# Performance work log

Hardware: AMD Instinct MI355X
Metric: run time of the kernel (lower is better)

## Reference

```python
import jax, jax.numpy as jnp
import numpy as np

N_NODES = 200000
N_GRAPHS = 4000


def _sage_conv(x, src, dst, W_l, b_l, W_r, num_nodes):
    # PyG SAGEConv (aggr='mean'): out = lin_l(mean_{j in N(i)} x_j) + lin_r(x_i)
    msg_sum = jax.ops.segment_sum(x[src], dst, num_segments=num_nodes)      # [N, d]
    deg = jax.ops.segment_sum(jnp.ones_like(src, dtype=x.dtype), dst,
                              num_segments=num_nodes)                       # [N]
    mean_nbr = msg_sum / jnp.maximum(deg, 1.0)[:, None]
    return mean_nbr @ W_l.T + b_l + x @ W_r.T


def setup_inputs() -> dict:
    key = jax.random.key(0)
    ks = jax.random.split(key, 10)
    in_ch, hid, out = 32, 64, 2
    E = 3200000
    x = jax.random.normal(ks[0], (N_NODES, in_ch), dtype=jnp.float32)
    edge_index = jax.random.randint(ks[1], (2, E), 0, N_NODES, dtype=jnp.int64)
    batch = jnp.sort(jax.random.randint(ks[2], (N_NODES,), 0, N_GRAPHS, dtype=jnp.int64))

    def glorot(k, shape):
        lim = 1.0 / np.sqrt(shape[1])
        return jax.random.uniform(k, shape, jnp.float32, -lim, lim)

    return {
        "x": x,
        "edge_index": edge_index,
        "batch": batch,
        "W1_l": glorot(ks[3], (hid, in_ch)),
        "b1": jnp.zeros((hid,), jnp.float32),
        "W1_r": glorot(ks[4], (hid, in_ch)),
        "W2_l": glorot(ks[5], (hid, hid)),
        "b2": jnp.zeros((hid,), jnp.float32),
        "W2_r": glorot(ks[6], (hid, hid)),
        "W_lin": glorot(ks[7], (out, hid)),
        "b_lin": jnp.zeros((out,), jnp.float32),
    }


def reference(x, edge_index, batch, W1_l, b1, W1_r, W2_l, b2, W2_r, W_lin, b_lin):
    src, dst = edge_index[0], edge_index[1]
    h = jax.nn.relu(_sage_conv(x, src, dst, W1_l, b1, W1_r, N_NODES))
    h = jax.nn.relu(_sage_conv(h, src, dst, W2_l, b2, W2_r, N_NODES))
    # global_mean_pool over graph ids
    pool_sum = jax.ops.segment_sum(h, batch, num_segments=N_GRAPHS)          # [G, 64]
    cnt = jax.ops.segment_sum(jnp.ones_like(batch, dtype=h.dtype), batch,
                              num_segments=N_GRAPHS)                          # [G]
    pooled = pool_sum / jnp.maximum(cnt, 1.0)[:, None]
    return pooled @ W_lin.T + b_lin
```

## Files before the change

### kernel.cpp

```cpp
#include <hip/hip_runtime.h>
#include <hip/hip_bf16.h>


#define WS_ALIGN 64
#define EPB 4096
#define BSHIFT 8
#define BNODES 256
#define BCAP 6144
#define MAXNB 1024

typedef short bf16x8 __attribute__((ext_vector_type(8)));
typedef float f32x4 __attribute__((ext_vector_type(4)));

__device__ inline unsigned short f2bf(float f) {
    unsigned u = __float_as_uint(f);
    return (unsigned short)((u + 0x7fffu + ((u >> 16) & 1u)) >> 16);
}

__device__ inline void acc8(const uint4 u, float* a) {
    a[0] += __uint_as_float(u.x << 16);
    a[1] += __uint_as_float(u.x & 0xffff0000u);
    a[2] += __uint_as_float(u.y << 16);
    a[3] += __uint_as_float(u.y & 0xffff0000u);
    a[4] += __uint_as_float(u.z << 16);
    a[5] += __uint_as_float(u.z & 0xffff0000u);
    a[6] += __uint_as_float(u.w << 16);
    a[7] += __uint_as_float(u.w & 0xffff0000u);
}


__global__ void prep_kernel(const float* __restrict__ x, unsigned short* __restrict__ xb,
                            const float* __restrict__ W1_l, const float* __restrict__ W1_r,
                            const float* __restrict__ W2_l, const float* __restrict__ W2_r,
                            unsigned short* __restrict__ whi1, unsigned short* __restrict__ whi2,
                            int* __restrict__ bucketCursor, float* __restrict__ pool,
                            int N, int NB, int G, int total4) {
    const int gid = blockIdx.x * blockDim.x + threadIdx.x;
    if (gid < total4) {
        const float4 v = reinterpret_cast<const float4*>(x)[gid];
        ushort4 o;
        o.x = f2bf(v.x); o.y = f2bf(v.y); o.z = f2bf(v.z); o.w = f2bf(v.w);
        reinterpret_cast<ushort4*>(xb)[gid] = o;
    }
    if (gid < NB) bucketCursor[gid] = gid * BCAP;
    if (gid < G * 64) pool[gid] = 0.0f;
    if (gid < 64 * 64) {
        const int o = gid >> 6, k = gid & 63;
        const float v = (k < 32) ? W1_l[o * 32 + k] : W1_r[o * 32 + (k - 32)];
        whi1[gid] = f2bf(v);
    }
    if (gid < 64 * 128) {
        const int o = gid >> 7, k = gid & 127;
        const float v = (k < 64) ? W2_l[o * 64 + k] : W2_r[o * 64 + (k - 64)];
        whi2[gid] = f2bf(v);
    }
}


__global__ __launch_bounds__(256) void bucket_scatter_kernel(const int* __restrict__ src,
                                                             const int* __restrict__ dst,
                                                             int* __restrict__ bucketCursor,
                                                             unsigned* __restrict__ bucketData,
                                                             int E, int NB) {
    __shared__ int hist[MAXNB];
    __shared__ int cur[MAXNB];
    const int t = threadIdx.x;
    for (int i = t; i < MAXNB; i += 256) hist[i] = 0;
    __syncthreads();
    const int eBase = blockIdx.x * EPB + t;
    int s[16], b[16], dl[16];
#pragma unroll
    for (int j = 0; j < 16; ++j) {
        int e = eBase + j * 256;
        if (e < E) {
            int d = dst[e];
            s[j]  = src[e];
            b[j]  = d >> BSHIFT;
            dl[j] = d & (BNODES - 1);
            atomicAdd(&hist[b[j]], 1);
        } else {
            b[j] = -1;
        }
    }
    __syncthreads();
    for (int bb = t; bb < NB; bb += 256)
        if (hist[bb] > 0) cur[bb] = atomicAdd(&bucketCursor[bb], hist[bb]);
    __syncthreads();
#pragma unroll
    for (int j = 0; j < 16; ++j) {
        if (b[j] >= 0) {
            int pos = atomicAdd(&cur[b[j]], 1);
            if (pos < (b[j] + 1) * BCAP)
                bucketData[pos] = ((unsigned)s[j] << BSHIFT) | (unsigned)dl[j];
        }
    }
}

__global__ __launch_bounds__(256) void csr_build_kernel(const unsigned* __restrict__ bucketData,
                                                        const int* __restrict__ bucketCursor,
                                                        int* __restrict__ offs,
                                                        int* __restrict__ offe,
                                                        int* __restrict__ csr_src,
                                                        int N) {
    __shared__ int cnt[BNODES];
    __shared__ int sscan[BNODES];
    __shared__ int cur[BNODES];
    const int t   = threadIdx.x;
    const int bkt = blockIdx.x;
    const int nodeBase = bkt << BSHIFT;
    const int regionBase = bkt * BCAP;
    const int count = min(bucketCursor[bkt] - regionBase, BCAP);
    cnt[t] = 0;
    __syncthreads();
    for (int k = regionBase + t; k < regionBase + count; k += 256)
        atomicAdd(&cnt[bucketData[k] & (BNODES - 1)], 1);
    __syncthreads();
    int v0 = cnt[t];
    sscan[t] = v0;
    __syncthreads();
    for (int off = 1; off < 256; off <<= 1) {
        int v = (t >= off) ? sscan[t - off] : 0;
        __syncthreads();
        sscan[t] += v;
        __syncthreads();
    }
    const int excl = sscan[t] - v0;
    cur[t] = excl;
    const int node = nodeBase + t;
    if (node < N) {
        offs[node] = regionBase + excl;
        offe[node] = regionBase + excl + v0;
    }
    __syncthreads();
    for (int k = regionBase + t; k < regionBase + count; k += 256) {
        const unsigned v = bucketData[k];
        const int d = (int)(v & (BNODES - 1));
        const int pos = regionBase + atomicAdd(&cur[d], 1);
        csr_src[pos] = (int)(v >> BSHIFT);
    }
}


template <int D>
__global__ void agg_bf16_kernel(const unsigned short* __restrict__ featb,
                                const int* __restrict__ csr_src,
                                const int* __restrict__ offs,
                                const int* __restrict__ offe,
                                unsigned short* __restrict__ aggb, int N) {
    constexpr int TPN = D / 8;
    int tid  = blockIdx.x * blockDim.x + threadIdx.x;
    int node = tid / TPN;
    int part = tid % TPN;
    if (node >= N) return;
    const int beg = offs[node];
    const int end = offe[node];
    const uint4* base = reinterpret_cast<const uint4*>(featb);
    float a[8] = {0.f, 0.f, 0.f, 0.f, 0.f, 0.f, 0.f, 0.f};
    int k = beg;
    for (; k + 8 <= end; k += 8) {
        int s[8];
#pragma unroll
        for (int j = 0; j < 8; ++j) s[j] = csr_src[k + j];
        uint4 u[8];
#pragma unroll
        for (int j = 0; j < 8; ++j) u[j] = base[(size_t)s[j] * TPN + part];
#pragma unroll
        for (int j = 0; j < 8; ++j) acc8(u[j], a);
    }
    for (; k + 4 <= end; k += 4) {
        const int s0 = csr_src[k + 0];
        const int s1 = csr_src[k + 1];
        const int s2 = csr_src[k + 2];
        const int s3 = csr_src[k + 3];
        const uint4 u0 = base[(size_t)s0 * TPN + part];
        const uint4 u1 = base[(size_t)s1 * TPN + part];
        const uint4 u2 = base[(size_t)s2 * TPN + part];
        const uint4 u3 = base[(size_t)s3 * TPN + part];
        acc8(u0, a); acc8(u1, a); acc8(u2, a); acc8(u3, a);
    }
    for (; k < end; ++k) {
        const uint4 u = base[(size_t)csr_src[k] * TPN + part];
        acc8(u, a);
    }
    const float inv = 1.0f / fmaxf((float)(end - beg), 1.0f);
    ushort4 lo, hi;
    lo.x = f2bf(a[0] * inv); lo.y = f2bf(a[1] * inv);
    lo.z = f2bf(a[2] * inv); lo.w = f2bf(a[3] * inv);
    hi.x = f2bf(a[4] * inv); hi.y = f2bf(a[5] * inv);
    hi.z = f2bf(a[6] * inv); hi.w = f2bf(a[7] * inv);
    unsigned short* dstp = aggb + (size_t)node * D + part * 8;
    *reinterpret_cast<ushort4*>(dstp)     = lo;
    *reinterpret_cast<ushort4*>(dstp + 4) = hi;
}


template <int DIN, bool POOL>
__launch_bounds__(256)
__global__ void mfma_dense_kernel(const unsigned short* __restrict__ aggb,
                                  const unsigned short* __restrict__ xinb,
                                  const unsigned short* __restrict__ whi,
                                  const float* __restrict__ bias,
                                  unsigned short* __restrict__ houtb,
                                  const int* __restrict__ batch,
                                  float* __restrict__ pool_sum,
                                  int N, int nSteps) {
    constexpr int K   = 2 * DIN;
    constexpr int STR = K + 8;
    constexpr int D8  = DIN / 8;
    constexpr int K8  = K / 8;
    __shared__ unsigned short A_s[64 * STR];
    __shared__ unsigned short Bh_s[64 * STR];
    const int tid = threadIdx.x;
    const int nodeBase = blockIdx.x * 64;

    for (int i = tid; i < 64 * D8 * 2; i += 256) {
        const int half = i / (64 * D8);
        const int j = i % (64 * D8);
        const int node = j / D8, q = j % D8;
        const int n = min(nodeBase + node, N - 1);
        const unsigned short* srcp = half ? xinb : aggb;
        const uint4 u = *reinterpret_cast<const uint4*>(srcp + (size_t)n * DIN + q * 8);
        *reinterpret_cast<uint4*>(&A_s[node * STR + half * DIN + q * 8]) = u;
    }
    for (int i = tid; i < 64 * K8; i += 256) {
        const int o = i / K8, q = i % K8;
        const uint4 u = *reinterpret_cast<const uint4*>(whi + (size_t)o * K + q * 8);
        *reinterpret_cast<uint4*>(&Bh_s[o * STR + q * 8]) = u;
    }
    __syncthreads();

    const int lane = tid & 63;
    const int wave = tid >> 6;
    const int lr = lane & 15;
    const int q  = lane >> 4;
    f32x4 acc[4];
#pragma unroll
    for (int t = 0; t < 4; ++t) {
        const float b = bias[t * 16 + lr];
        acc[t] = (f32x4){b, b, b, b};
    }
    const unsigned short* Arow = &A_s[(wave * 16 + lr) * STR + q * 8];
    for (int s = 0; s < nSteps; ++s) {
        const bf16x8 af = *reinterpret_cast<const bf16x8*>(Arow + s * 32);
#pragma unroll
        for (int t = 0; t < 4; ++t) {
            const bf16x8 bh = *reinterpret_cast<const bf16x8*>(
                &Bh_s[(t * 16 + lr) * STR + s * 32 + q * 8]);
            acc[t] = __builtin_amdgcn_mfma_f32_16x16x32_bf16(af, bh, acc[t], 0, 0, 0);
        }
    }

    if (POOL) {
        float ag[4] = {0.f, 0.f, 0.f, 0.f};
        int gcur = -1;
        for (int reg = 0; reg < 4; ++reg) {
            const int n = nodeBase + wave * 16 + q * 4 + reg;
            if (n >= N) break;
            const int g = batch[n];
            if (g != gcur) {
                if (gcur >= 0) {
#pragma unroll
                    for (int t = 0; t < 4; ++t)
                        atomicAdd(&pool_sum[(size_t)gcur * 64 + t * 16 + lr], ag[t]);
                }
                gcur = g;
                ag[0] = ag[1] = ag[2] = ag[3] = 0.f;
            }
#pragma unroll
            for (int t = 0; t < 4; ++t)
                ag[t] += fmaxf(acc[t][reg], 0.0f);
        }
        if (gcur >= 0) {
#pragma unroll
            for (int t = 0; t < 4; ++t)
                atomicAdd(&pool_sum[(size_t)gcur * 64 + t * 16 + lr], ag[t]);
        }
    } else {
        for (int reg = 0; reg < 4; ++reg) {
            const int n = nodeBase + wave * 16 + q * 4 + reg;
            if (n >= N) break;
#pragma unroll
            for (int t = 0; t < 4; ++t)
                houtb[(size_t)n * 64 + t * 16 + lr] = f2bf(fmaxf(acc[t][reg], 0.0f));
        }
    }
}


__device__ inline int lower_bound_batch(const int* __restrict__ batch, int N, int key) {
    int lo = 0, hi = N;
    while (lo < hi) {
        const int mid = (lo + hi) >> 1;
        if (batch[mid] < key) lo = mid + 1; else hi = mid;
    }
    return lo;
}

__global__ void final_kernel(const float* __restrict__ pool_sum,
                             const int* __restrict__ batch,
                             const float* __restrict__ W_lin,
                             const float* __restrict__ b_lin,
                             float* __restrict__ out, int G, int N) {
    int t = blockIdx.x * blockDim.x + threadIdx.x;
    if (t >= G * 2) return;
    int g = t >> 1, o = t & 1;
    const int c0 = lower_bound_batch(batch, N, g);
    const int c1 = lower_bound_batch(batch, N, g + 1);
    float inv = 1.0f / fmaxf((float)(c1 - c0), 1.0f);
    float acc = b_lin[o];
#pragma unroll
    for (int c = 0; c < 64; ++c)
        acc = fmaf(pool_sum[(size_t)g * 64 + c] * inv, W_lin[o * 64 + c], acc);
    out[t] = acc;
}

extern "C" void kernel_launch(void* const* d_in, const int* in_sizes, int n_in,
                              void* d_out, int out_size, void* d_ws, size_t ws_size,
                              hipStream_t stream) {
    const float* x     = (const float*)d_in[0];
    const int*   ei    = (const int*)d_in[1];
    const int*   batch = (const int*)d_in[2];
    const float* W1_l  = (const float*)d_in[3];
    const float* b1    = (const float*)d_in[4];
    const float* W1_r  = (const float*)d_in[5];
    const float* W2_l  = (const float*)d_in[6];
    const float* b2    = (const float*)d_in[7];
    const float* W2_r  = (const float*)d_in[8];
    const float* W_lin = (const float*)d_in[9];
    const float* b_lin = (const float*)d_in[10];

    const int N = in_sizes[0] / 32;
    const int E = in_sizes[1] / 2;
    const int G = out_size / 2;
    const int* src = ei;
    const int* dst = ei + E;
    const int NB = (N + BNODES - 1) >> BSHIFT;

    char* p = (char*)d_ws;
    auto carve = [&](size_t bytes) -> void* {
        void* r = (void*)p;
        p += (bytes + (WS_ALIGN - 1)) / WS_ALIGN * WS_ALIGN;
        return r;
    };
    int*            bucketCursor = (int*)carve((size_t)MAXNB * 4);
    unsigned*       bucketData   = (unsigned*)carve((size_t)NB * BCAP * 4);
    int*            offs         = (int*)carve((size_t)N * 4);
    int*            offe         = (int*)carve((size_t)N * 4);
    int*            csr_src      = (int*)carve((size_t)NB * BCAP * 4);
    unsigned short* xb           = (unsigned short*)carve((size_t)N * 32 * 2);
    unsigned short* aggb         = (unsigned short*)carve((size_t)N * 64 * 2);
    unsigned short* h1b          = (unsigned short*)carve((size_t)N * 64 * 2);
    unsigned short* whi1         = (unsigned short*)carve(64 * 64 * 2);
    unsigned short* whi2         = (unsigned short*)carve(64 * 128 * 2);
    float*          pool         = (float*)carve((size_t)G * 64 * 4);
    float*          out          = (float*)d_out;

    const int TB = 256;
    const int total4 = N * 32 / 4;
    prep_kernel<<<(total4 + TB - 1) / TB, TB, 0, stream>>>(
        x, xb, W1_l, W1_r, W2_l, W2_r, whi1, whi2, bucketCursor, pool,
        N, NB, G, total4);
    bucket_scatter_kernel<<<(E + EPB - 1) / EPB, TB, 0, stream>>>(src, dst, bucketCursor,
                                                                  bucketData, E, NB);
    csr_build_kernel<<<NB, TB, 0, stream>>>(bucketData, bucketCursor, offs, offe, csr_src, N);

    agg_bf16_kernel<32><<<((size_t)N * 4 + TB - 1) / TB, TB, 0, stream>>>(
        xb, csr_src, offs, offe, aggb, N);
    mfma_dense_kernel<32, false><<<(N + 63) / 64, TB, 0, stream>>>(
        aggb, xb, whi1, b1, h1b, nullptr, nullptr, N, 2);

    agg_bf16_kernel<64><<<((size_t)N * 8 + TB - 1) / TB, TB, 0, stream>>>(
        h1b, csr_src, offs, offe, aggb, N);
    mfma_dense_kernel<64, true><<<(N + 63) / 64, TB, 0, stream>>>(
        aggb, h1b, whi2, b2, nullptr, batch, pool, N, 4);

    final_kernel<<<(G * 2 + TB - 1) / TB, TB, 0, stream>>>(pool, batch, W_lin, b_lin,
                                                           out, G, N);
}
```

Baseline: 357.7 us.

## Double CSR bucket size and edges per scatter block, re-read edges instead of caching

Bucket width grows from 256 to 512 nodes, which halves the number of buckets and csr_build blocks. Each scatter block now handles 8192 edges. The scatter kernel no longer keeps per-edge values in registers: it reloads dst and src from global memory in the second pass, trading extra memory reads for lower register pressure. csr_build now covers two nodes per thread with a paired prefix scan. Larger buckets mean more per-block work and more contention on the shared-memory atomics.

```diff
diff --git a/kernel.cpp b/kernel.cpp
--- a/kernel.cpp
+++ b/kernel.cpp
@@ -3,11 +3,11 @@
 
 
 #define WS_ALIGN 64
-#define EPB 4096
-#define BSHIFT 8
-#define BNODES 256
-#define BCAP 6144
-#define MAXNB 1024
+#define EPB 8192
+#define BSHIFT 9
+#define BNODES 512
+#define BCAP 11264
+#define MAXNB 512
 
 typedef short bf16x8 __attribute__((ext_vector_type(8)));
 typedef float f32x4 __attribute__((ext_vector_type(4)));
@@ -65,33 +65,27 @@
     __shared__ int hist[MAXNB];
     __shared__ int cur[MAXNB];
     const int t = threadIdx.x;
-    for (int i = t; i < MAXNB; i += 256) hist[i] = 0;
+    for (int i = t; i < NB; i += 256) hist[i] = 0;
     __syncthreads();
     const int eBase = blockIdx.x * EPB + t;
-    int s[16], b[16], dl[16];
-#pragma unroll
-    for (int j = 0; j < 16; ++j) {
-        int e = eBase + j * 256;
-        if (e < E) {
-            int d = dst[e];
-            s[j]  = src[e];
-            b[j]  = d >> BSHIFT;
-            dl[j] = d & (BNODES - 1);
-            atomicAdd(&hist[b[j]], 1);
-        } else {
-            b[j] = -1;
-        }
+#pragma unroll 4
+    for (int j = 0; j < 32; ++j) {
+        const int e = eBase + j * 256;
+        if (e < E) atomicAdd(&hist[dst[e] >> BSHIFT], 1);
     }
     __syncthreads();
     for (int bb = t; bb < NB; bb += 256)
         if (hist[bb] > 0) cur[bb] = atomicAdd(&bucketCursor[bb], hist[bb]);
     __syncthreads();
-#pragma unroll
-    for (int j = 0; j < 16; ++j) {
-        if (b[j] >= 0) {
-            int pos = atomicAdd(&cur[b[j]], 1);
-            if (pos < (b[j] + 1) * BCAP)
-                bucketData[pos] = ((unsigned)s[j] << BSHIFT) | (unsigned)dl[j];
+#pragma unroll 4
+    for (int j = 0; j < 32; ++j) {
+        const int e = eBase + j * 256;
+        if (e < E) {
+            const int d = dst[e];
+            const int b = d >> BSHIFT;
+            const int pos = atomicAdd(&cur[b], 1);
+            if (pos < (b + 1) * BCAP)
+                bucketData[pos] = ((unsigned)src[e] << BSHIFT) | (unsigned)(d & (BNODES - 1));
         }
     }
 }
@@ -103,20 +97,22 @@
                                                         int* __restrict__ csr_src,
                                                         int N) {
     __shared__ int cnt[BNODES];
-    __shared__ int sscan[BNODES];
+    __shared__ int sscan[256];
     __shared__ int cur[BNODES];
     const int t   = threadIdx.x;
     const int bkt = blockIdx.x;
     const int nodeBase = bkt << BSHIFT;
     const int regionBase = bkt * BCAP;
     const int count = min(bucketCursor[bkt] - regionBase, BCAP);
-    cnt[t] = 0;
+    cnt[t] = 0; cnt[t + 256] = 0;
     __syncthreads();
     for (int k = regionBase + t; k < regionBase + count; k += 256)
         atomicAdd(&cnt[bucketData[k] & (BNODES - 1)], 1);
     __syncthreads();
-    int v0 = cnt[t];
-    sscan[t] = v0;
+    const int c0 = cnt[2 * t];
+    const int c1 = cnt[2 * t + 1];
+    const int sum = c0 + c1;
+    sscan[t] = sum;
     __syncthreads();
     for (int off = 1; off < 256; off <<= 1) {
         int v = (t >= off) ? sscan[t - off] : 0;
@@ -124,13 +120,13 @@
         sscan[t] += v;
         __syncthreads();
     }
-    const int excl = sscan[t] - v0;
-    cur[t] = excl;
-    const int node = nodeBase + t;
-    if (node < N) {
-        offs[node] = regionBase + excl;
-        offe[node] = regionBase + excl + v0;
-    }
+    const int base = sscan[t] - sum;
+    cur[2 * t]     = base;
+    cur[2 * t + 1] = base + c0;
+    const int n0 = nodeBase + 2 * t;
+    const int n1 = n0 + 1;
+    if (n0 < N) { offs[n0] = regionBase + base;      offe[n0] = regionBase + base + c0; }
+    if (n1 < N) { offs[n1] = regionBase + base + c0; offe[n1] = regionBase + base + c0 + c1; }
     __syncthreads();
     for (int k = regionBase + t; k < regionBase + count; k += 256) {
         const unsigned v = bucketData[k];
```

Result: slower. 368.5 us (+3.0%).
